# Performance work log

Hardware: AMD Instinct MI355X
Metric: run time of the kernel (lower is better)

Reference implementation:

```python
import jax, jax.numpy as jnp
import numpy as np

FEATURE_DIM = 128

def setup_inputs() -> dict:
    key0 = jax.random.key(0)
    k1, k2, k3 = jax.random.split(key0, 3)
    B, NQ, NK, D = 4, 4096, 4096, FEATURE_DIM
    return {
        "target": jax.random.normal(k1, (B, NQ, D), dtype=jnp.float32),
        "key": jax.random.normal(k2, (B, NK, D), dtype=jnp.float32),
        "value": jax.random.normal(k3, (B, NK, D), dtype=jnp.float32),
    }

def reference(target, key, value):
    # Lan_K F: scores = target @ key^T / sqrt(d); weights = softmax(scores); out = weights @ value
    scale = 1.0 / np.sqrt(FEATURE_DIM).astype(np.float32)
    scores = jnp.einsum('bqd,bkd->bqk', target, key) * scale  # [B, NQ, NK]
    weights = jax.nn.softmax(scores, axis=-1)
    return jnp.einsum('bqk,bkd->bqd', weights, value)  # [B, NQ, D]
```

## Files before the change

### kernel.cpp

```cpp
#include <hip/hip_runtime.h>
#include <stdint.h>

#define B_ 4
#define NQ_ 4096
#define NK_ 4096
#define D_ 128
#define BM_ 64
#define BN_ 128
#define NITER_ (NK_/BN_)
#define PS_ 136
#define OS_ 66

typedef __attribute__((ext_vector_type(8))) short short8;
typedef __attribute__((ext_vector_type(4))) float floatx4;
typedef unsigned int u32;

union frag_u { u32 u[4]; short8 s; };
union pair_u { u32 u[2]; uint2 v; };

__device__ __forceinline__ unsigned short f2bf_rne(float x){
  union { float f; u32 u; } c; c.f = x;
  u32 u = c.u;
  return (unsigned short)((u + 0x7fffu + ((u >> 16) & 1u)) >> 16);
}
__device__ __forceinline__ u32 pk2bf(float a, float b){
  union { float f; u32 u; } x, y; x.f = a; y.f = b;
  return ((x.u + 0x8000u) >> 16) | ((y.u + 0x8000u) & 0xffff0000u);
}

#define TS_ 136
__global__ void prep_kernel(const float* __restrict__ k, const float* __restrict__ v,
                            unsigned short* __restrict__ kf, unsigned short* __restrict__ vf){
  if (blockIdx.x >= 256){
    int base = (blockIdx.x - 256) * 1024 + threadIdx.x;
    #pragma unroll
    for (int i = 0; i < 4; i++){
      int flat = base + i*256;
      int lane = flat & 63, j = (flat>>6)&3, w = (flat>>8)&7;
      int it = (flat>>11)&31, b = flat>>16;
      int kg = w>>1, dh = w&1, l15 = lane&15, l4 = lane>>4;
      int key = it*128 + kg*32 + ((l15>>2)<<3) + dh*4 + (l15&3);
      int d0 = j*32 + l4*8;
      const float* p = k + ((size_t)b*NK_ + key)*D_ + d0;
      float4 a = *(const float4*)p;
      float4 c = *(const float4*)(p + 4);
      ushort4 s0, s1;
      s0.x = f2bf_rne(a.x); s0.y = f2bf_rne(a.y);
      s0.z = f2bf_rne(a.z); s0.w = f2bf_rne(a.w);
      s1.x = f2bf_rne(c.x); s1.y = f2bf_rne(c.y);
      s1.z = f2bf_rne(c.z); s1.w = f2bf_rne(c.w);
      ushort4* dst = (ushort4*)(kf + (size_t)flat*8);
      dst[0] = s0; dst[1] = s1;
    }
    return;
  }
  __shared__ __align__(16) float tile[64*TS_];
  int blk = blockIdx.x; int b = blk >> 6; int kt = blk & 63; int k0 = kt*64;
  int it = kt >> 1; int khalf = (kt & 1) * 64;
  int t = threadIdx.x;
  const float* vb = v + ((size_t)b*NK_ + k0)*D_;
  #pragma unroll
  for (int i=0;i<8;i++){
    int f = t + i*256;
    int row = f >> 5, c4 = f & 31;
    *(float4*)(tile + row*TS_ + c4*4) = *(const float4*)(vb + row*D_ + c4*4);
  }
  __syncthreads();
  #pragma unroll
  for (int i=0;i<16;i++){
    int u2 = t + i*256;
    int d = u2 >> 5, kp = u2 & 31;
    int klocal = khalf + 2*kp;
    int kg = klocal >> 5, l4 = (klocal >> 3) & 3, ko7 = klocal & 7;
    int dh = d >> 6, dt = (d >> 4) & 3, l15 = d & 15;
    int w = kg*2 + dh, lane = l4*16 + l15;
    size_t flat = ((((size_t)b*32 + it)*8 + w)*4 + dt)*64 + lane;
    ushort2 s2;
    s2.x = f2bf_rne(tile[(2*kp)*TS_ + d]);
    s2.y = f2bf_rne(tile[(2*kp+1)*TS_ + d]);
    *(ushort2*)(vf + flat*8 + ko7) = s2;
  }
}

__global__ __launch_bounds__(512, 2) void attn_kernel(
    const float* __restrict__ Qf, const unsigned short* __restrict__ Kb,
    const unsigned short* __restrict__ Vt, float* __restrict__ Out){
  __shared__ __align__(16) char sm[69632];
  unsigned short* smP = (unsigned short*)sm;
  float* smO = (float*)sm;
  float* smL = (float*)(sm + 67584);

  const int bi = blockIdx.x;
  const int b  = (bi >> 1) & 3;
  const int qt = ((bi >> 3) << 1) | (bi & 1);
  const int q0 = qt * BM_;
  const int tid = threadIdx.x;
  const int w = tid >> 6, lane = tid & 63;
  const int kg = w >> 1, dh = w & 1;
  const int l15 = lane & 15, l4 = lane >> 4;

  const short8* Kfrag = (const short8*)Kb;
  const short8* Vfrag = (const short8*)Vt;
  const size_t FSTRIDE = 8*4*64;
  const size_t fbase = (((size_t)b*32)*8 + w)*4*64 + lane;

  short8 kf[4], knf[4];
  #pragma unroll
  for (int j = 0; j < 4; j++) kf[j] = Kfrag[fbase + j*64];

  short8 qf[4][4];
  {
    const float* qp = Qf + ((size_t)b*NQ_ + q0)*D_;
    #pragma unroll
    for (int nb = 0; nb < 4; nb++)
      #pragma unroll
      for (int kb = 0; kb < 4; kb++){
        const float* p = qp + (size_t)(nb*16 + l15)*D_ + kb*32 + l4*8;
        float4 a = *(const float4*)p;
        float4 c4 = *(const float4*)(p + 4);
        frag_u f;
        f.u[0] = pk2bf(a.x, a.y);  f.u[1] = pk2bf(a.z, a.w);
        f.u[2] = pk2bf(c4.x, c4.y); f.u[3] = pk2bf(c4.z, c4.w);
        qf[nb][kb] = f.s;
      }
  }

  floatx4 o[4][4];
  #pragma unroll
  for (int nb = 0; nb < 4; nb++)
    #pragma unroll
    for (int dt = 0; dt < 4; dt++) o[nb][dt] = (floatx4)0.0f;
  float lsum[4] = {0.f, 0.f, 0.f, 0.f};

  const float SL = 0.08838834764831845f * 1.4426950408889634f;

  for (int it = 0; it < NITER_; ++it){
    short8 vf[4];
    #pragma unroll
    for (int dt = 0; dt < 4; dt++)
      vf[dt] = Vfrag[fbase + (size_t)it*FSTRIDE + dt*64];
    if (it + 1 < NITER_){
      #pragma unroll
      for (int j = 0; j < 4; j++)
        knf[j] = Kfrag[fbase + (size_t)(it+1)*FSTRIDE + j*64];
    }

    floatx4 s[4];
    #pragma unroll
    for (int nb = 0; nb < 4; nb++){
      s[nb] = (floatx4)0.0f;
      s[nb] = __builtin_amdgcn_mfma_f32_16x16x32_bf16(kf[0], qf[nb][0], s[nb], 0,0,0);
      s[nb] = __builtin_amdgcn_mfma_f32_16x16x32_bf16(kf[1], qf[nb][1], s[nb], 0,0,0);
      s[nb] = __builtin_amdgcn_mfma_f32_16x16x32_bf16(kf[2], qf[nb][2], s[nb], 0,0,0);
      s[nb] = __builtin_amdgcn_mfma_f32_16x16x32_bf16(kf[3], qf[nb][3], s[nb], 0,0,0);
    }

    unsigned short* smPb = smP + (it & 1) * (64 * PS_);
    #pragma unroll
    for (int nb = 0; nb < 4; nb++){
      float p0 = __builtin_amdgcn_exp2f(s[nb][0] * SL);
      float p1 = __builtin_amdgcn_exp2f(s[nb][1] * SL);
      float p2 = __builtin_amdgcn_exp2f(s[nb][2] * SL);
      float p3 = __builtin_amdgcn_exp2f(s[nb][3] * SL);
      lsum[nb] += (p0 + p1) + (p2 + p3);
      pair_u pp; pp.u[0] = pk2bf(p0, p1); pp.u[1] = pk2bf(p2, p3);
      *(uint2*)(smPb + (size_t)(nb*16 + l15)*PS_ + kg*32 + l4*8 + dh*4) = pp.v;
    }

    __syncthreads();

    short8 pf[4];
    #pragma unroll
    for (int nb = 0; nb < 4; nb++)
      pf[nb] = *(const short8*)(smPb + (size_t)(nb*16 + l15)*PS_ + kg*32 + l4*8);
    #pragma unroll
    for (int nb = 0; nb < 4; nb++)
      #pragma unroll
      for (int dt = 0; dt < 4; dt++)
        o[nb][dt] = __builtin_amdgcn_mfma_f32_16x16x32_bf16(pf[nb], vf[dt], o[nb][dt], 0,0,0);

    #pragma unroll
    for (int j = 0; j < 4; j++) kf[j] = knf[j];
  }

  #pragma unroll
  for (int nb = 0; nb < 4; nb++){
    float v = lsum[nb];
    v += __shfl_xor(v, 16);
    v += __shfl_xor(v, 32);
    lsum[nb] = v;
  }
  if (l4 == 0)
    #pragma unroll
    for (int nb = 0; nb < 4; nb++)
      smL[w*64 + nb*16 + l15] = lsum[nb];

  __syncthreads();

  if (w >= 4){
    float* r = smO + (size_t)(w - 4) * 4224;
    #pragma unroll
    for (int nb = 0; nb < 4; nb++)
      #pragma unroll
      for (int dt = 0; dt < 4; dt++)
        #pragma unroll
        for (int q = 0; q < 4; q++)
          r[(size_t)(nb*16 + l4*4 + q)*OS_ + dt*16 + l15] = o[nb][dt][q];
  }
  __syncthreads();
  if (w < 4){
    float* r = smO + (size_t)w * 4224;
    #pragma unroll
    for (int nb = 0; nb < 4; nb++)
      #pragma unroll
      for (int dt = 0; dt < 4; dt++)
        #pragma unroll
        for (int q = 0; q < 4; q++)
          o[nb][dt][q] += r[(size_t)(nb*16 + l4*4 + q)*OS_ + dt*16 + l15];
  }
  __syncthreads();
  if (w == 2 || w == 3){
    float* r = smO + (size_t)(w - 2) * 4224;
    #pragma unroll
    for (int nb = 0; nb < 4; nb++)
      #pragma unroll
      for (int dt = 0; dt < 4; dt++)
        #pragma unroll
        for (int q = 0; q < 4; q++)
          r[(size_t)(nb*16 + l4*4 + q)*OS_ + dt*16 + l15] = o[nb][dt][q];
  }
  __syncthreads();
  if (w < 2){
    float* r = smO + (size_t)w * 4224;
    float* og = Out + ((size_t)b*NQ_ + q0)*D_ + dh*64;
    #pragma unroll
    for (int nb = 0; nb < 4; nb++)
      #pragma unroll
      for (int q = 0; q < 4; q++){
        int row = nb*16 + l4*4 + q;
        float lt = 0.f;
        #pragma unroll
        for (int w2 = 0; w2 < 8; w2++) lt += smL[w2*64 + row];
        float inv = 1.0f / lt;
        #pragma unroll
        for (int dt = 0; dt < 4; dt++){
          float val = o[nb][dt][q] + r[(size_t)row*OS_ + dt*16 + l15];
          og[(size_t)row*D_ + dt*16 + l15] = val * inv;
        }
      }
  }
}

extern "C" void kernel_launch(void* const* d_in, const int* in_sizes, int n_in,
                              void* d_out, int out_size, void* d_ws, size_t ws_size,
                              hipStream_t stream){
  const float* q = (const float*)d_in[0];
  const float* k = (const float*)d_in[1];
  const float* v = (const float*)d_in[2];
  float* out = (float*)d_out;
  unsigned short* kb = (unsigned short*)d_ws;
  unsigned short* vt = kb + (size_t)B_*NK_*D_;
  prep_kernel<<<512, 256, 0, stream>>>(k, v, kb, vt);
  attn_kernel<<<256, 512, 0, stream>>>(q, kb, vt, out);
}
```

Measured before the change: 120.5 us.

## Double-buffer K/V register fragments with two-deep prefetch and lighter barriers

The attention loop is unrolled by two and keeps two register sets of K and V fragments, prefetching tiles two iterations ahead instead of one. __syncthreads is replaced by an explicit lgkmcnt wait plus s_barrier, so outstanding global loads are not drained at each barrier. The V prep kernel is restructured so each thread writes a full 16-byte fragment instead of scattered 4-byte pieces. The aim is to hide global load latency behind MFMA work, at the cost of more VGPRs under a 512x2 launch bound, which risks spills.

```diff
diff --git a/kernel.cpp b/kernel.cpp
--- a/kernel.cpp
+++ b/kernel.cpp
@@ -56,7 +56,7 @@
   }
   __shared__ __align__(16) float tile[64*TS_];
   int blk = blockIdx.x; int b = blk >> 6; int kt = blk & 63; int k0 = kt*64;
-  int it = kt >> 1; int khalf = (kt & 1) * 64;
+  int it = kt >> 1; int kgbase = (kt & 1) * 2;
   int t = threadIdx.x;
   const float* vb = v + ((size_t)b*NK_ + k0)*D_;
   #pragma unroll
@@ -66,19 +66,26 @@
     *(float4*)(tile + row*TS_ + c4*4) = *(const float4*)(vb + row*D_ + c4*4);
   }
   __syncthreads();
-  #pragma unroll
-  for (int i=0;i<16;i++){
-    int u2 = t + i*256;
-    int d = u2 >> 5, kp = u2 & 31;
-    int klocal = khalf + 2*kp;
-    int kg = klocal >> 5, l4 = (klocal >> 3) & 3, ko7 = klocal & 7;
-    int dh = d >> 6, dt = (d >> 4) & 3, l15 = d & 15;
-    int w = kg*2 + dh, lane = l4*16 + l15;
+  int lane = t & 63, dt = t >> 6;
+  int l4 = lane >> 4, l15 = lane & 15;
+  #pragma unroll
+  for (int i = 0; i < 4; i++){
+    int kg_loc = i >> 1, dh = i & 1;
+    int w = (kgbase + kg_loc)*2 + dh;
+    int d = dh*64 + dt*16 + l15;
+    int r0 = kg_loc*32 + l4*8;
     size_t flat = ((((size_t)b*32 + it)*8 + w)*4 + dt)*64 + lane;
-    ushort2 s2;
-    s2.x = f2bf_rne(tile[(2*kp)*TS_ + d]);
-    s2.y = f2bf_rne(tile[(2*kp+1)*TS_ + d]);
-    *(ushort2*)(vf + flat*8 + ko7) = s2;
+    ushort4 s0, s1;
+    s0.x = f2bf_rne(tile[(r0+0)*TS_ + d]);
+    s0.y = f2bf_rne(tile[(r0+1)*TS_ + d]);
+    s0.z = f2bf_rne(tile[(r0+2)*TS_ + d]);
+    s0.w = f2bf_rne(tile[(r0+3)*TS_ + d]);
+    s1.x = f2bf_rne(tile[(r0+4)*TS_ + d]);
+    s1.y = f2bf_rne(tile[(r0+5)*TS_ + d]);
+    s1.z = f2bf_rne(tile[(r0+6)*TS_ + d]);
+    s1.w = f2bf_rne(tile[(r0+7)*TS_ + d]);
+    ushort4* dst = (ushort4*)(vf + flat*8);
+    dst[0] = s0; dst[1] = s1;
   }
 }
 
@@ -104,10 +111,6 @@
   const size_t FSTRIDE = 8*4*64;
   const size_t fbase = (((size_t)b*32)*8 + w)*4*64 + lane;
 
-  short8 kf[4], knf[4];
-  #pragma unroll
-  for (int j = 0; j < 4; j++) kf[j] = Kfrag[fbase + j*64];
-
   short8 qf[4][4];
   {
     const float* qp = Qf + ((size_t)b*NQ_ + q0)*D_;
@@ -125,6 +128,16 @@
       }
   }
 
+  short8 kfA[4], kfB[4], vfA[4], vfB[4];
+  #pragma unroll
+  for (int j = 0; j < 4; j++) kfA[j] = Kfrag[fbase + j*64];
+  #pragma unroll
+  for (int dt = 0; dt < 4; dt++) vfA[dt] = Vfrag[fbase + dt*64];
+  #pragma unroll
+  for (int j = 0; j < 4; j++) kfB[j] = Kfrag[fbase + FSTRIDE + j*64];
+  #pragma unroll
+  for (int dt = 0; dt < 4; dt++) vfB[dt] = Vfrag[fbase + FSTRIDE + dt*64];
+
   floatx4 o[4][4];
   #pragma unroll
   for (int nb = 0; nb < 4; nb++)
@@ -133,54 +146,97 @@
   float lsum[4] = {0.f, 0.f, 0.f, 0.f};
 
   const float SL = 0.08838834764831845f * 1.4426950408889634f;
-
-  for (int it = 0; it < NITER_; ++it){
-    short8 vf[4];
-    #pragma unroll
-    for (int dt = 0; dt < 4; dt++)
-      vf[dt] = Vfrag[fbase + (size_t)it*FSTRIDE + dt*64];
-    if (it + 1 < NITER_){
-      #pragma unroll
-      for (int j = 0; j < 4; j++)
-        knf[j] = Kfrag[fbase + (size_t)(it+1)*FSTRIDE + j*64];
+  const size_t prow = (size_t)kg*32 + l4*8;
+
+  for (int it = 0; it < NITER_; it += 2){
+    {
+      floatx4 s[4];
+      #pragma unroll
+      for (int nb = 0; nb < 4; nb++){
+        s[nb] = (floatx4)0.0f;
+        s[nb] = __builtin_amdgcn_mfma_f32_16x16x32_bf16(kfA[0], qf[nb][0], s[nb], 0,0,0);
+        s[nb] = __builtin_amdgcn_mfma_f32_16x16x32_bf16(kfA[1], qf[nb][1], s[nb], 0,0,0);
+        s[nb] = __builtin_amdgcn_mfma_f32_16x16x32_bf16(kfA[2], qf[nb][2], s[nb], 0,0,0);
+        s[nb] = __builtin_amdgcn_mfma_f32_16x16x32_bf16(kfA[3], qf[nb][3], s[nb], 0,0,0);
+      }
+      if (it + 2 < NITER_){
+        #pragma unroll
+        for (int j = 0; j < 4; j++)
+          kfA[j] = Kfrag[fbase + (size_t)(it+2)*FSTRIDE + j*64];
+      }
+      unsigned short* smPb = smP;
+      #pragma unroll
+      for (int nb = 0; nb < 4; nb++){
+        float p0 = __builtin_amdgcn_exp2f(s[nb][0] * SL);
+        float p1 = __builtin_amdgcn_exp2f(s[nb][1] * SL);
+        float p2 = __builtin_amdgcn_exp2f(s[nb][2] * SL);
+        float p3 = __builtin_amdgcn_exp2f(s[nb][3] * SL);
+        lsum[nb] += (p0 + p1) + (p2 + p3);
+        pair_u pp; pp.u[0] = pk2bf(p0, p1); pp.u[1] = pk2bf(p2, p3);
+        *(uint2*)(smPb + (size_t)(nb*16 + l15)*PS_ + prow + dh*4) = pp.v;
+      }
+      asm volatile("s_waitcnt lgkmcnt(0)" ::: "memory");
+      __builtin_amdgcn_s_barrier();
+      asm volatile("" ::: "memory");
+      short8 pf[4];
+      #pragma unroll
+      for (int nb = 0; nb < 4; nb++)
+        pf[nb] = *(const short8*)(smPb + (size_t)(nb*16 + l15)*PS_ + prow);
+      #pragma unroll
+      for (int nb = 0; nb < 4; nb++)
+        #pragma unroll
+        for (int dt = 0; dt < 4; dt++)
+          o[nb][dt] = __builtin_amdgcn_mfma_f32_16x16x32_bf16(pf[nb], vfA[dt], o[nb][dt], 0,0,0);
+      if (it + 2 < NITER_){
+        #pragma unroll
+        for (int dt = 0; dt < 4; dt++)
+          vfA[dt] = Vfrag[fbase + (size_t)(it+2)*FSTRIDE + dt*64];
+      }
     }
-
-    floatx4 s[4];
-    #pragma unroll
-    for (int nb = 0; nb < 4; nb++){
-      s[nb] = (floatx4)0.0f;
-      s[nb] = __builtin_amdgcn_mfma_f32_16x16x32_bf16(kf[0], qf[nb][0], s[nb], 0,0,0);
-      s[nb] = __builtin_amdgcn_mfma_f32_16x16x32_bf16(kf[1], qf[nb][1], s[nb], 0,0,0);
-      s[nb] = __builtin_amdgcn_mfma_f32_16x16x32_bf16(kf[2], qf[nb][2], s[nb], 0,0,0);
-      s[nb] = __builtin_amdgcn_mfma_f32_16x16x32_bf16(kf[3], qf[nb][3], s[nb], 0,0,0);
+    {
+      floatx4 s[4];
+      #pragma unroll
+      for (int nb = 0; nb < 4; nb++){
+        s[nb] = (floatx4)0.0f;
+        s[nb] = __builtin_amdgcn_mfma_f32_16x16x32_bf16(kfB[0], qf[nb][0], s[nb], 0,0,0);
+        s[nb] = __builtin_amdgcn_mfma_f32_16x16x32_bf16(kfB[1], qf[nb][1], s[nb], 0,0,0);
+        s[nb] = __builtin_amdgcn_mfma_f32_16x16x32_bf16(kfB[2], qf[nb][2], s[nb], 0,0,0);
+        s[nb] = __builtin_amdgcn_mfma_f32_16x16x32_bf16(kfB[3], qf[nb][3], s[nb], 0,0,0);
+      }
+      if (it + 3 < NITER_){
+        #pragma unroll
+        for (int j = 0; j < 4; j++)
+          kfB[j] = Kfrag[fbase + (size_t)(it+3)*FSTRIDE + j*64];
+      }
+      unsigned short* smPb = smP + 64*PS_;
+      #pragma unroll
+      for (int nb = 0; nb < 4; nb++){
+        float p0 = __builtin_amdgcn_exp2f(s[nb][0] * SL);
+        float p1 = __builtin_amdgcn_exp2f(s[nb][1] * SL);
+        float p2 = __builtin_amdgcn_exp2f(s[nb][2] * SL);
+        float p3 = __builtin_amdgcn_exp2f(s[nb][3] * SL);
+        lsum[nb] += (p0 + p1) + (p2 + p3);
+        pair_u pp; pp.u[0] = pk2bf(p0, p1); pp.u[1] = pk2bf(p2, p3);
+        *(uint2*)(smPb + (size_t)(nb*16 + l15)*PS_ + prow + dh*4) = pp.v;
+      }
+      asm volatile("s_waitcnt lgkmcnt(0)" ::: "memory");
+      __builtin_amdgcn_s_barrier();
+      asm volatile("" ::: "memory");
+      short8 pf[4];
+      #pragma unroll
+      for (int nb = 0; nb < 4; nb++)
+        pf[nb] = *(const short8*)(smPb + (size_t)(nb*16 + l15)*PS_ + prow);
+      #pragma unroll
+      for (int nb = 0; nb < 4; nb++)
+        #pragma unroll
+        for (int dt = 0; dt < 4; dt++)
+          o[nb][dt] = __builtin_amdgcn_mfma_f32_16x16x32_bf16(pf[nb], vfB[dt], o[nb][dt], 0,0,0);
+      if (it + 3 < NITER_){
+        #pragma unroll
+        for (int dt = 0; dt < 4; dt++)
+          vfB[dt] = Vfrag[fbase + (size_t)(it+3)*FSTRIDE + dt*64];
+      }
     }
-
-    unsigned short* smPb = smP + (it & 1) * (64 * PS_);
-    #pragma unroll
-    for (int nb = 0; nb < 4; nb++){
-      float p0 = __builtin_amdgcn_exp2f(s[nb][0] * SL);
-      float p1 = __builtin_amdgcn_exp2f(s[nb][1] * SL);
-      float p2 = __builtin_amdgcn_exp2f(s[nb][2] * SL);
-      float p3 = __builtin_amdgcn_exp2f(s[nb][3] * SL);
-      lsum[nb] += (p0 + p1) + (p2 + p3);
-      pair_u pp; pp.u[0] = pk2bf(p0, p1); pp.u[1] = pk2bf(p2, p3);
-      *(uint2*)(smPb + (size_t)(nb*16 + l15)*PS_ + kg*32 + l4*8 + dh*4) = pp.v;
-    }
-
-    __syncthreads();
-
-    short8 pf[4];
-    #pragma unroll
-    for (int nb = 0; nb < 4; nb++)
-      pf[nb] = *(const short8*)(smPb + (size_t)(nb*16 + l15)*PS_ + kg*32 + l4*8);
-    #pragma unroll
-    for (int nb = 0; nb < 4; nb++)
-      #pragma unroll
-      for (int dt = 0; dt < 4; dt++)
-        o[nb][dt] = __builtin_amdgcn_mfma_f32_16x16x32_bf16(pf[nb], vf[dt], o[nb][dt], 0,0,0);
-
-    #pragma unroll
-    for (int j = 0; j < 4; j++) kf[j] = knf[j];
   }
 
   #pragma unroll
```

Result: faster. 117.0 us (-2.9%).
